# Kernel tuning notes

Measured on AMD Instinct MI355X. Metric: run time of the kernel, lower is better.

## Reference

```python
import jax, jax.numpy as jnp
import numpy as np

# Irrep layout: 512x0e + 512x1o + 512x2e  (dims 512*1, 512*3, 512*5)
MUL = 512
LS = (0, 1, 2)


def setup_inputs() -> dict:
    key = jax.random.key(0)
    k1, k2, k3, k4 = jax.random.split(key, 4)
    N = 16384
    dim = MUL * sum(2 * l + 1 for l in LS)  # 4608
    x1 = jax.random.normal(k1, (N, dim), dtype=jnp.float32)
    x2 = jnp.ones((N, 1), dtype=jnp.float32)  # trivial 1x0e input of e3nn Linear
    W0 = jax.random.normal(k2, (MUL, 1, MUL), dtype=jnp.float32)
    W1 = jax.random.normal(k3, (MUL, 1, MUL), dtype=jnp.float32)
    W2 = jax.random.normal(k4, (MUL, 1, MUL), dtype=jnp.float32)
    return {"x1": x1, "x2": x2, "W0": W0, "W1": W1, "W2": W2}


def reference(x1, x2, W0, W1, W2):
    N = x1.shape[0]
    # path normalization: c = sqrt(alpha * path_weight / (mul_1 * mul_2)),
    # alpha = 1 (single path per output, unit variances), mul_2 = 1
    c = 1.0 / jnp.sqrt(jnp.asarray(MUL, dtype=x1.dtype))
    parts = []
    off = 0
    for W, l in ((W0, 0), (W1, 1), (W2, 2)):
        d = 2 * l + 1
        s1 = x1[:, off:off + MUL * d].reshape(N, MUL, d)  # [N, u, i]
        # specialized codegen branch (l2=0, l1=l_out, uvw):
        # out = c * einsum('uvw,zui,zv->zwi', ws, s1, s2)
        y = c * jnp.einsum('uvw,zui,zv->zwi', W, s1, x2)  # [N, w, i]
        parts.append(y.reshape(N, MUL * d))
        off += MUL * d
    return jnp.concatenate(parts, axis=1)
```

## Files before the change

### kernel.cpp

```cpp
#include <hip/hip_runtime.h>
#include <stdint.h>

typedef float f32x4 __attribute__((ext_vector_type(4)));
typedef __bf16 bf16x8 __attribute__((ext_vector_type(8)));

#define DIM 4608
#define BK 64
#define NT 8
#define WS_L_BYTES (16 * 4 * 512 * 16)

#define BARLGKM()                                \
  do {                                           \
    __builtin_amdgcn_sched_barrier(0);           \
    asm volatile("s_waitcnt lgkmcnt(0)" ::: "memory"); \
    __builtin_amdgcn_s_barrier();                \
    __builtin_amdgcn_sched_barrier(0);           \
  } while (0)

__global__ __launch_bounds__(256) void prepack(const float* __restrict__ W0,
                                               const float* __restrict__ W1,
                                               const float* __restrict__ W2,
                                               char* __restrict__ ws) {
  int gid = blockIdx.x * 256 + threadIdx.x;
  int col = gid & 511;
  int rest = gid >> 9;
  int grp = rest & 3;
  rest >>= 2;
  int t = rest & 15;
  int l = rest >> 4;
  const float* W = (l == 0) ? W0 : ((l == 1) ? W1 : W2);
  const float c = 0.044194173824159216f;
  union {
    bf16x8 v;
    uint4 u;
  } pk;
#pragma unroll
  for (int jj = 0; jj < 8; ++jj) {
    float v = W[(t * 32 + grp * 8 + jj) * 512 + col] * c;
    pk.v[jj] = (__bf16)v;
  }
  *(uint4*)(ws + (size_t)l * WS_L_BYTES + ((size_t)((t * 4 + grp) * 512 + col) << 4)) = pk.u;
}

template <int D, int BZ, int OFF>
__device__ __forceinline__ void gemm_body(int zc, int j, const float* __restrict__ x1,
                                          const float* __restrict__ x2,
                                          const char* __restrict__ wsl,
                                          float* __restrict__ out,
                                          char* __restrict__ smem) {
  constexpr int BM = BZ * D;
  constexpr int R = BM / 16;
  constexpr int RAWB = BZ * BK * D * 4;
  constexpr int CH = RAWB / 16;
  constexpr int CPR = BK * D / 4;
  constexpr int UNITS = BM * (BK / 8);
  constexpr int KD = (CH + 511) / 512;
  constexpr int KU = (UNITS + 511) / 512;

  char* rawbuf = smem;
  char* fragbuf = smem + 2 * RAWB;

  const int tid = threadIdx.x;
  const int z0 = zc * BZ;
  const int cb = j * 256;
  const float* xbase = x1 + (size_t)z0 * DIM + OFF;

  const int lane = tid & 63;
  const int wave = tid >> 6;
  const int llo = lane & 15;
  const int lhi = lane >> 4;

  const float* gsrc[KD];
#pragma unroll
  for (int k = 0; k < KD; ++k) {
    int c = tid + k * 512;
    int rowz = c / CPR;
    int off = c - rowz * CPR;
    gsrc[k] = xbase + (size_t)rowz * DIM + off * 4;
  }

  f32x4 acc[R][2];
#pragma unroll
  for (int rt = 0; rt < R; ++rt)
#pragma unroll
    for (int ct = 0; ct < 2; ++ct) acc[rt][ct] = (f32x4){0.f, 0.f, 0.f, 0.f};

  auto dma = [&](int t) {
    char* ldst = rawbuf + (t & 1) * RAWB;
    const int tof = t * (BK * D);
#pragma unroll
    for (int k = 0; k < KD; ++k) {
      int c = tid + k * 512;
      if ((CH % 512 == 0) || (c < CH)) {
        __builtin_amdgcn_global_load_lds(
            (const __attribute__((address_space(1))) uint32_t*)(gsrc[k] + tof),
            (__attribute__((address_space(3))) uint32_t*)(ldst + (size_t)c * 16), 16, 0, 0);
      }
    }
  };

  auto repack = [&](int t) {
    const float* raw = (const float*)(rawbuf + (t & 1) * RAWB);
#pragma unroll
    for (int s = 0; s < KU; ++s) {
      int u = tid + s * 512;
      if ((UNITS % 512 == 0) || (u < UNITS)) {
        int kg = u / BM;
        int r = u - kg * BM;
        int z = r / D;
        int i = r - z * D;
        const float* base = raw + z * (BK * D) + (kg * 8) * D + i;
        bf16x8 v;
#pragma unroll
        for (int jj = 0; jj < 8; ++jj) v[jj] = (__bf16)base[jj * D];
        *(bf16x8*)(fragbuf + (size_t)u * 16) = v;
      }
    }
  };

  auto load_b = [&](bf16x8 (&b)[2][2], int t) {
#pragma unroll
    for (int kk = 0; kk < 2; ++kk)
#pragma unroll
      for (int ct = 0; ct < 2; ++ct)
        b[kk][ct] = *(const bf16x8*)(wsl + ((size_t)(((2 * t + kk) * 4 + lhi) * 512 + cb +
                                                    wave * 32 + ct * 16 + llo)
                                            << 4));
  };

  auto compute = [&](bf16x8 (&b)[2][2]) {
#pragma unroll
    for (int kk = 0; kk < 2; ++kk)
#pragma unroll
      for (int rt = 0; rt < R; ++rt) {
        bf16x8 af =
            *(const bf16x8*)(fragbuf + (((kk * 4 + lhi) * BM + rt * 16 + llo) << 4));
#pragma unroll
        for (int ct = 0; ct < 2; ++ct)
          acc[rt][ct] = __builtin_amdgcn_mfma_f32_16x16x32_bf16(af, b[kk][ct], acc[rt][ct], 0, 0, 0);
      }
  };

  dma(0);
#pragma unroll 2
  for (int t = 0; t < NT; ++t) {
    __syncthreads();
    if (t + 1 < NT) dma(t + 1);
    bf16x8 b[2][2];
    load_b(b, t);
    repack(t);
    BARLGKM();
    compute(b);
  }

  float* obase = out + (size_t)z0 * DIM + OFF;
#pragma unroll
  for (int rt = 0; rt < R; ++rt) {
#pragma unroll
    for (int reg = 0; reg < 4; ++reg) {
      int row = rt * 16 + lhi * 4 + reg;
      int z = row / D;
      int i = row - z * D;
      float s = x2[z0 + z];
#pragma unroll
      for (int ct = 0; ct < 2; ++ct) {
        int col = cb + wave * 32 + ct * 16 + llo;
        obase[(size_t)z * DIM + col * D + i] = acc[rt][ct][reg] * s;
      }
    }
  }
}

__global__ __launch_bounds__(512, 4) void gemm_fused(const float* __restrict__ x1,
                                                     const float* __restrict__ x2,
                                                     const char* __restrict__ ws,
                                                     float* __restrict__ out) {
  __shared__ __align__(16) char smem[51200];
  int bid = blockIdx.x;
  if (bid < 2048) {
    gemm_body<5, 16, 2048>(bid >> 1, bid & 1, x1, x2, ws + 2 * (size_t)WS_L_BYTES, out, smem);
  } else if (bid < 4096) {
    int b = bid - 2048;
    gemm_body<3, 16, 512>(b >> 1, b & 1, x1, x2, ws + (size_t)WS_L_BYTES, out, smem);
  } else {
    int b = bid - 4096;
    gemm_body<1, 64, 0>(b >> 1, b & 1, x1, x2, ws, out, smem);
  }
}

extern "C" void kernel_launch(void* const* d_in, const int* in_sizes, int n_in,
                              void* d_out, int out_size, void* d_ws, size_t ws_size,
                              hipStream_t stream) {
  const float* x1 = (const float*)d_in[0];
  const float* x2 = (const float*)d_in[1];
  const float* W0 = (const float*)d_in[2];
  const float* W1 = (const float*)d_in[3];
  const float* W2 = (const float*)d_in[4];
  float* out = (float*)d_out;
  char* ws = (char*)d_ws;

  prepack<<<384, 256, 0, stream>>>(W0, W1, W2, ws);
  gemm_fused<<<4608, 512, 0, stream>>>(x1, x2, ws, out);
}
```

Before: 235.2 us.

## Shrink blocks to 256 threads, halve K tile, swizzle LDS, prefetch B

```diff
diff --git a/kernel.cpp b/kernel.cpp
--- a/kernel.cpp
+++ b/kernel.cpp
@@ -5,16 +5,24 @@
 typedef __bf16 bf16x8 __attribute__((ext_vector_type(8)));
 
 #define DIM 4608
-#define BK 64
-#define NT 8
+#define BK 32
+#define NT 16
 #define WS_L_BYTES (16 * 4 * 512 * 16)
 
-#define BARLGKM()                                \
-  do {                                           \
-    __builtin_amdgcn_sched_barrier(0);           \
-    asm volatile("s_waitcnt lgkmcnt(0)" ::: "memory"); \
-    __builtin_amdgcn_s_barrier();                \
-    __builtin_amdgcn_sched_barrier(0);           \
+#define ENTRY()                                         \
+  do {                                                  \
+    __builtin_amdgcn_sched_barrier(0);                  \
+    asm volatile("s_waitcnt vmcnt(2)" ::: "memory");    \
+    __builtin_amdgcn_s_barrier();                       \
+    __builtin_amdgcn_sched_barrier(0);                  \
+  } while (0)
+
+#define LGKMBAR()                                       \
+  do {                                                  \
+    __builtin_amdgcn_sched_barrier(0);                  \
+    asm volatile("s_waitcnt lgkmcnt(0)" ::: "memory");  \
+    __builtin_amdgcn_s_barrier();                       \
+    __builtin_amdgcn_sched_barrier(0);                  \
   } while (0)
 
 __global__ __launch_bounds__(256) void prepack(const float* __restrict__ W0,
@@ -54,15 +62,15 @@
   constexpr int CH = RAWB / 16;
   constexpr int CPR = BK * D / 4;
   constexpr int UNITS = BM * (BK / 8);
-  constexpr int KD = (CH + 511) / 512;
-  constexpr int KU = (UNITS + 511) / 512;
+  constexpr int KD = (CH + 255) / 256;
+  constexpr int KU = (UNITS + 255) / 256;
 
   char* rawbuf = smem;
   char* fragbuf = smem + 2 * RAWB;
 
   const int tid = threadIdx.x;
   const int z0 = zc * BZ;
-  const int cb = j * 256;
+  const int cb = j * 128;
   const float* xbase = x1 + (size_t)z0 * DIM + OFF;
 
   const int lane = tid & 63;
@@ -70,15 +78,6 @@
   const int llo = lane & 15;
   const int lhi = lane >> 4;
 
-  const float* gsrc[KD];
-#pragma unroll
-  for (int k = 0; k < KD; ++k) {
-    int c = tid + k * 512;
-    int rowz = c / CPR;
-    int off = c - rowz * CPR;
-    gsrc[k] = xbase + (size_t)rowz * DIM + off * 4;
-  }
-
   f32x4 acc[R][2];
 #pragma unroll
   for (int rt = 0; rt < R; ++rt)
@@ -87,70 +86,84 @@
 
   auto dma = [&](int t) {
     char* ldst = rawbuf + (t & 1) * RAWB;
-    const int tof = t * (BK * D);
+    const float* xs = xbase + t * (BK * D);
 #pragma unroll
     for (int k = 0; k < KD; ++k) {
-      int c = tid + k * 512;
-      if ((CH % 512 == 0) || (c < CH)) {
+      int c = tid + k * 256;
+      if ((CH % 256 == 0) || (c < CH)) {
+        int g = c ^ ((c / CPR) & 7);
+        int rowz = g / CPR;
+        int off = g - rowz * CPR;
         __builtin_amdgcn_global_load_lds(
-            (const __attribute__((address_space(1))) uint32_t*)(gsrc[k] + tof),
+            (const __attribute__((address_space(1))) uint32_t*)(xs + (size_t)rowz * DIM + off * 4),
             (__attribute__((address_space(3))) uint32_t*)(ldst + (size_t)c * 16), 16, 0, 0);
       }
     }
   };
 
   auto repack = [&](int t) {
-    const float* raw = (const float*)(rawbuf + (t & 1) * RAWB);
+    const char* rawt = rawbuf + (t & 1) * RAWB;
 #pragma unroll
     for (int s = 0; s < KU; ++s) {
-      int u = tid + s * 512;
-      if ((UNITS % 512 == 0) || (u < UNITS)) {
+      int u = tid + s * 256;
+      if ((UNITS % 256 == 0) || (u < UNITS)) {
         int kg = u / BM;
         int r = u - kg * BM;
         int z = r / D;
         int i = r - z * D;
-        const float* base = raw + z * (BK * D) + (kg * 8) * D + i;
         bf16x8 v;
 #pragma unroll
-        for (int jj = 0; jj < 8; ++jj) v[jj] = (__bf16)base[jj * D];
+        for (int jj = 0; jj < 8; ++jj) {
+          int fb = (kg * 8 + jj) * D + i;
+          int b = z * (CPR * 16) + fb * 4;
+          int lb = ((((b >> 4) ^ (z & 7)) << 4) | (b & 15));
+          v[jj] = (__bf16)(*(const float*)(rawt + lb));
+        }
         *(bf16x8*)(fragbuf + (size_t)u * 16) = v;
       }
     }
   };
 
-  auto load_b = [&](bf16x8 (&b)[2][2], int t) {
-#pragma unroll
-    for (int kk = 0; kk < 2; ++kk)
+  auto load_b = [&](bf16x8 (&b)[2], int t) {
+    const char* wt = wsl + (size_t)t * 32768;
+#pragma unroll
+    for (int ct = 0; ct < 2; ++ct)
+      b[ct] = *(const bf16x8*)(wt + ((lhi * 512 + cb + wave * 32 + ct * 16 + llo) << 4));
+  };
+
+  auto compute = [&](bf16x8 (&b)[2]) {
+#pragma unroll
+    for (int rt = 0; rt < R; ++rt) {
+      bf16x8 af = *(const bf16x8*)(fragbuf + ((lhi * BM + rt * 16 + llo) << 4));
 #pragma unroll
       for (int ct = 0; ct < 2; ++ct)
-        b[kk][ct] = *(const bf16x8*)(wsl + ((size_t)(((2 * t + kk) * 4 + lhi) * 512 + cb +
-                                                    wave * 32 + ct * 16 + llo)
-                                            << 4));
-  };
-
-  auto compute = [&](bf16x8 (&b)[2][2]) {
-#pragma unroll
-    for (int kk = 0; kk < 2; ++kk)
-#pragma unroll
-      for (int rt = 0; rt < R; ++rt) {
-        bf16x8 af =
-            *(const bf16x8*)(fragbuf + (((kk * 4 + lhi) * BM + rt * 16 + llo) << 4));
-#pragma unroll
-        for (int ct = 0; ct < 2; ++ct)
-          acc[rt][ct] = __builtin_amdgcn_mfma_f32_16x16x32_bf16(af, b[kk][ct], acc[rt][ct], 0, 0, 0);
-      }
-  };
-
+        acc[rt][ct] = __builtin_amdgcn_mfma_f32_16x16x32_bf16(af, b[ct], acc[rt][ct], 0, 0, 0);
+    }
+  };
+
+  bf16x8 bE[2], bO[2];
   dma(0);
-#pragma unroll 2
-  for (int t = 0; t < NT; ++t) {
-    __syncthreads();
-    if (t + 1 < NT) dma(t + 1);
-    bf16x8 b[2][2];
-    load_b(b, t);
+  __builtin_amdgcn_sched_barrier(0);
+  load_b(bE, 0);
+
+  for (int tt = 0; tt < NT / 2; ++tt) {
+    const int t = 2 * tt;
+    ENTRY();
+    dma(t + 1);
+    __builtin_amdgcn_sched_barrier(0);
+    load_b(bO, t + 1);
     repack(t);
-    BARLGKM();
-    compute(b);
+    LGKMBAR();
+    compute(bE);
+    ENTRY();
+    if (tt < NT / 2 - 1) {
+      dma(t + 2);
+      __builtin_amdgcn_sched_barrier(0);
+      load_b(bE, t + 2);
+    }
+    repack(t + 1);
+    LGKMBAR();
+    compute(bO);
   }
 
   float* obase = out + (size_t)z0 * DIM + OFF;
@@ -171,20 +184,20 @@
   }
 }
 
-__global__ __launch_bounds__(512, 4) void gemm_fused(const float* __restrict__ x1,
+__global__ __launch_bounds__(256, 5) void gemm_fused(const float* __restrict__ x1,
                                                      const float* __restrict__ x2,
                                                      const char* __restrict__ ws,
                                                      float* __restrict__ out) {
-  __shared__ __align__(16) char smem[51200];
+  __shared__ __align__(16) char smem[25600];
   int bid = blockIdx.x;
-  if (bid < 2048) {
-    gemm_body<5, 16, 2048>(bid >> 1, bid & 1, x1, x2, ws + 2 * (size_t)WS_L_BYTES, out, smem);
-  } else if (bid < 4096) {
-    int b = bid - 2048;
-    gemm_body<3, 16, 512>(b >> 1, b & 1, x1, x2, ws + (size_t)WS_L_BYTES, out, smem);
+  if (bid < 4096) {
+    gemm_body<5, 16, 2048>(bid >> 2, bid & 3, x1, x2, ws + 2 * (size_t)WS_L_BYTES, out, smem);
+  } else if (bid < 8192) {
+    int b = bid - 4096;
+    gemm_body<3, 16, 512>(b >> 2, b & 3, x1, x2, ws + (size_t)WS_L_BYTES, out, smem);
   } else {
-    int b = bid - 4096;
-    gemm_body<1, 64, 0>(b >> 1, b & 1, x1, x2, ws, out, smem);
+    int b = bid - 8192;
+    gemm_body<1, 64, 0>(b >> 2, b & 3, x1, x2, ws, out, smem);
   }
 }
 
@@ -200,5 +213,5 @@
   char* ws = (char*)d_ws;
 
   prepack<<<384, 256, 0, stream>>>(W0, W1, W2, ws);
-  gemm_fused<<<4608, 512, 0, stream>>>(x1, x2, ws, out);
-}
+  gemm_fused<<<9216, 256, 0, stream>>>(x1, x2, ws, out);
+}
```

Result: slower. 381.7 us (+62.3%).
